# Kernel optimization log

Measured on AMD Instinct MI355X. Metric: run time of the kernel, lower is better.

Reference implementation:

```python
import jax, jax.numpy as jnp
import numpy as np
import math

MAX_ITERATIONS = 10
CONVERGENCE_EPS = 1e-6
B, L = 2048, 2048


def quaternion_normalize(q):
    return q / (jnp.linalg.norm(q, axis=-1, keepdims=True) + 1e-12)


def hamilton_product(q1, q2):
    w1, x1, y1, z1 = q1[..., 0], q1[..., 1], q1[..., 2], q1[..., 3]
    w2, x2, y2, z2 = q2[..., 0], q2[..., 1], q2[..., 2], q2[..., 3]
    return jnp.stack([
        w1 * w2 - x1 * x2 - y1 * y2 - z1 * z2,
        w1 * x2 + x1 * w2 + y1 * z2 - z1 * y2,
        w1 * y2 - x1 * z2 + y1 * w2 + z1 * x2,
        w1 * z2 + x1 * y2 - y1 * x2 + z1 * w2,
    ], axis=-1)


def quaternion_log(q):
    # log map on S^3 at identity
    w = jnp.clip(q[..., 0], -1.0 + 1e-7, 1.0 - 1e-7)
    v = q[..., 1:]
    theta = jnp.arccos(w)
    sin_theta = jnp.sin(theta)[..., None] + 1e-9
    return theta[..., None] / sin_theta * v


def quaternion_exp(v):
    theta = jnp.linalg.norm(v, axis=-1, keepdims=True)
    v_n = v / (theta + 1e-9)
    return jnp.concatenate([jnp.cos(theta), jnp.sin(theta) * v_n], axis=-1)


def compute_karcher_mean(points):
    # points: [N, B, L, 4] unit quaternions
    n = points.shape[0]
    weights = jnp.full((n,), 1.0 / n, dtype=points.dtype)
    conj = jnp.asarray([1.0, -1.0, -1.0, -1.0], dtype=points.dtype)

    def step(carry, _):
        mu, done = carry
        mu_inv = mu * conj
        q_rel = hamilton_product(mu_inv[None], points)      # [N, B, L, 4]
        tangent = quaternion_log(q_rel)                     # [N, B, L, 3]
        mean_v = jnp.sum(tangent * weights[:, None, None, None], axis=0)
        delta_mu = quaternion_exp(mean_v)
        mu_new = quaternion_normalize(hamilton_product(mu, delta_mu))
        # torch: update mu, then break if ||mean_v|| < eps -> freeze afterward
        mu_out = jnp.where(done, mu, mu_new)
        new_done = done | (jnp.linalg.norm(mean_v) < CONVERGENCE_EPS)
        return (mu_out, new_done), None

    mu0 = points[0]
    (mu, _), _ = jax.lax.scan(step, (mu0, jnp.asarray(False)), None, length=MAX_ITERATIONS)
    return mu


def calculate_spectral_shift(barycenter):
    w, x, y, z = (barycenter[..., 0], barycenter[..., 1],
                  barycenter[..., 2], barycenter[..., 3])
    # S = [[w+iz, x+iy], [-x+iy, w-iz]] ; det(S) = (w+iz)(w-iz) - (x+iy)(-x+iy)
    s00 = jax.lax.complex(w, z)
    s01 = jax.lax.complex(x, y)
    s10 = jax.lax.complex(-x, y)
    s11 = jax.lax.complex(w, -z)
    det_s = s00 * s11 - s01 * s10
    return jnp.angle(det_s) / math.pi


def setup_inputs() -> dict:
    key = jax.random.key(0)
    ks = jax.random.split(key, 4)
    names = ['audio', 'vision', 'text', 'genomic']
    return {n: jax.random.normal(k, (B, L, 4), dtype=jnp.float32)
            for n, k in zip(names, ks)}


def reference(audio, vision, text, genomic):
    stacked = jnp.stack([quaternion_normalize(audio),
                         quaternion_normalize(vision),
                         quaternion_normalize(text),
                         quaternion_normalize(genomic)], axis=0)  # [4, B, L, 4]
    barycenter = compute_karcher_mean(stacked)
    eta = calculate_spectral_shift(barycenter)
    curvature = jnp.linalg.norm(barycenter - quaternion_normalize(barycenter))
    veracity = 1.0 / (1.0 + curvature)
    return barycenter, eta, veracity
```

## Files before the change

### kernel.cpp

```cpp
#include <hip/hip_runtime.h>


#define NPTS (2048 * 2048)
#define NBLK (NPTS / 256)

__device__ __forceinline__ float frcp(float x) { return __builtin_amdgcn_rcpf(x); }
__device__ __forceinline__ float frsq(float x) { return __builtin_amdgcn_rsqf(x); }
__device__ __forceinline__ float fsqrt(float x) { return __builtin_amdgcn_sqrtf(x); }

__device__ __forceinline__ float4 qnorm_fast(const float4 q) {
    float inv = frsq(fmaf(q.x, q.x, fmaf(q.y, q.y, fmaf(q.z, q.z, q.w * q.w))));
    return make_float4(q.x * inv, q.y * inv, q.z * inv, q.w * inv);
}

__device__ __forceinline__ float log_scale(float w) {
    float a = fminf(fabsf(w), 0.9999999f);
    float t = fmaf(a, fmaf(a, fmaf(a, -0.004682325f, 0.018565250f), -0.053028600f),
                   0.392682200f);
    float r1 = frsq(1.0f + a);
    float r2 = frsq(1.0f - a);
    float u = fmaf(0.785398163f, r2, -t);
    return r1 * ((w >= 0.0f) ? t : u);
}

__device__ __forceinline__ float sinc_poly(float x) {
    float s = fmaf(x, 1.60590438e-10f, -2.50521084e-8f);
    s = fmaf(x, s, 2.75573192e-6f);
    s = fmaf(x, s, -1.98412698e-4f);
    s = fmaf(x, s, 8.33333333e-3f);
    s = fmaf(x, s, -1.66666667e-1f);
    return fmaf(x, s, 1.0f);
}
__device__ __forceinline__ float cos_poly(float x) {
    float c = fmaf(x, -1.14707456e-11f, 2.08767570e-9f);
    c = fmaf(x, c, -2.75573192e-7f);
    c = fmaf(x, c, 2.48015873e-5f);
    c = fmaf(x, c, -1.38888889e-3f);
    c = fmaf(x, c, 4.16666667e-2f);
    c = fmaf(x, c, -0.5f);
    return fmaf(x, c, 1.0f);
}

__global__ __launch_bounds__(256) void karcher_kernel(
    const float4* __restrict__ aud, const float4* __restrict__ vis,
    const float4* __restrict__ txt, const float4* __restrict__ gen,
    float* __restrict__ out, float* __restrict__ ws)
{
    const int i = blockIdx.x * 256 + threadIdx.x;

    float4 p0 = qnorm_fast(aud[i]);
    float4 p1 = qnorm_fast(vis[i]);
    float4 p2 = qnorm_fast(txt[i]);
    float4 p3 = qnorm_fast(gen[i]);

    float4 mu = p0;

    #pragma unroll
    for (int it = 0; it < 10; ++it) {
        float w0 = fmaf(mu.x, p0.x, fmaf(mu.y, p0.y, fmaf(mu.z, p0.z, mu.w * p0.w)));
        float w1 = fmaf(mu.x, p1.x, fmaf(mu.y, p1.y, fmaf(mu.z, p1.z, mu.w * p1.w)));
        float w2 = fmaf(mu.x, p2.x, fmaf(mu.y, p2.y, fmaf(mu.z, p2.z, mu.w * p2.w)));
        float w3 = fmaf(mu.x, p3.x, fmaf(mu.y, p3.y, fmaf(mu.z, p3.z, mu.w * p3.w)));

        float s0 = log_scale(w0), s1 = log_scale(w1), s2 = log_scale(w2), s3 = log_scale(w3);

        float Tw = fmaf(s0, p0.x, fmaf(s1, p1.x, fmaf(s2, p2.x, s3 * p3.x)));
        float Tx = fmaf(s0, p0.y, fmaf(s1, p1.y, fmaf(s2, p2.y, s3 * p3.y)));
        float Ty = fmaf(s0, p0.z, fmaf(s1, p1.z, fmaf(s2, p2.z, s3 * p3.z)));
        float Tz = fmaf(s0, p0.w, fmaf(s1, p1.w, fmaf(s2, p2.w, s3 * p3.w)));

        float d  = fmaf(mu.x, Tw, fmaf(mu.y, Tx, fmaf(mu.z, Ty, mu.w * Tz)));
        float Ew = fmaf(-d, mu.x, Tw);
        float Ex = fmaf(-d, mu.y, Tx);
        float Ey = fmaf(-d, mu.z, Ty);
        float Ez = fmaf(-d, mu.w, Tz);
        float x  = fmaf(Ew, Ew, fmaf(Ex, Ex, fmaf(Ey, Ey, Ez * Ez)));

        float sc = sinc_poly(x);
        float c  = cos_poly(x);
        mu.x = fmaf(c, mu.x, sc * Ew);
        mu.y = fmaf(c, mu.y, sc * Ex);
        mu.z = fmaf(c, mu.z, sc * Ey);
        mu.w = fmaf(c, mu.w, sc * Ez);
    }

    mu = qnorm_fast(mu);

    reinterpret_cast<float4*>(out)[i] = mu;

    out[4 * NPTS + i] = 0.0f;

    float nn = fmaf(mu.x, mu.x, fmaf(mu.y, mu.y, fmaf(mu.z, mu.z, mu.w * mu.w)));
    float invn = frcp(fsqrt(nn) + 1e-12f);
    float ex = fmaf(-mu.x, invn, mu.x);
    float ey = fmaf(-mu.y, invn, mu.y);
    float ez = fmaf(-mu.z, invn, mu.z);
    float ew = fmaf(-mu.w, invn, mu.w);
    float ss = fmaf(ex, ex, fmaf(ey, ey, fmaf(ez, ez, ew * ew)));

    #pragma unroll
    for (int off = 32; off > 0; off >>= 1)
        ss += __shfl_down(ss, off, 64);
    __shared__ float part[4];
    if ((threadIdx.x & 63) == 0) part[threadIdx.x >> 6] = ss;
    __syncthreads();
    if (threadIdx.x == 0)
        ws[blockIdx.x] = part[0] + part[1] + part[2] + part[3];
}

__global__ __launch_bounds__(256) void finish_kernel(
    const float* __restrict__ ws, float* __restrict__ out)
{
    float s = 0.0f;
    #pragma unroll 4
    for (int k = threadIdx.x; k < NBLK; k += 256)
        s += ws[k];
    #pragma unroll
    for (int off = 32; off > 0; off >>= 1)
        s += __shfl_down(s, off, 64);
    __shared__ float part[4];
    if ((threadIdx.x & 63) == 0) part[threadIdx.x >> 6] = s;
    __syncthreads();
    if (threadIdx.x == 0)
        out[5 * NPTS] = 1.0f / (1.0f + sqrtf(part[0] + part[1] + part[2] + part[3]));
}

extern "C" void kernel_launch(void* const* d_in, const int* in_sizes, int n_in,
                              void* d_out, int out_size, void* d_ws, size_t ws_size,
                              hipStream_t stream) {
    const float4* aud = (const float4*)d_in[0];
    const float4* vis = (const float4*)d_in[1];
    const float4* txt = (const float4*)d_in[2];
    const float4* gen = (const float4*)d_in[3];
    float* out = (float*)d_out;
    float* ws = (float*)d_ws;

    karcher_kernel<<<NBLK, 256, 0, stream>>>(aud, vis, txt, gen, out, ws);
    finish_kernel<<<1, 256, 0, stream>>>(ws, out);
}
```

Before: 145.2 us.

## Process two points per thread, peel first iteration, reuse dot products for tangent projection

```diff
diff --git a/kernel.cpp b/kernel.cpp
--- a/kernel.cpp
+++ b/kernel.cpp
@@ -2,7 +2,7 @@
 
 
 #define NPTS (2048 * 2048)
-#define NBLK (NPTS / 256)
+#define NBLK (NPTS / 512)
 
 __device__ __forceinline__ float frcp(float x) { return __builtin_amdgcn_rcpf(x); }
 __device__ __forceinline__ float frsq(float x) { return __builtin_amdgcn_rsqf(x); }
@@ -41,62 +41,88 @@
     return fmaf(x, c, 1.0f);
 }
 
+__device__ __forceinline__ float4 karcher_update(
+    float4 mu, float s0, float w0,
+    const float4 p0, const float4 p1, const float4 p2, const float4 p3)
+{
+    float w1 = fmaf(mu.x, p1.x, fmaf(mu.y, p1.y, fmaf(mu.z, p1.z, mu.w * p1.w)));
+    float w2 = fmaf(mu.x, p2.x, fmaf(mu.y, p2.y, fmaf(mu.z, p2.z, mu.w * p2.w)));
+    float w3 = fmaf(mu.x, p3.x, fmaf(mu.y, p3.y, fmaf(mu.z, p3.z, mu.w * p3.w)));
+    float s1 = log_scale(w1), s2 = log_scale(w2), s3 = log_scale(w3);
+
+    float Tw = fmaf(s0, p0.x, fmaf(s1, p1.x, fmaf(s2, p2.x, s3 * p3.x)));
+    float Tx = fmaf(s0, p0.y, fmaf(s1, p1.y, fmaf(s2, p2.y, s3 * p3.y)));
+    float Ty = fmaf(s0, p0.z, fmaf(s1, p1.z, fmaf(s2, p2.z, s3 * p3.z)));
+    float Tz = fmaf(s0, p0.w, fmaf(s1, p1.w, fmaf(s2, p2.w, s3 * p3.w)));
+
+    float d = fmaf(s0, w0, fmaf(s1, w1, fmaf(s2, w2, s3 * w3)));
+
+    float Ew = fmaf(-d, mu.x, Tw);
+    float Ex = fmaf(-d, mu.y, Tx);
+    float Ey = fmaf(-d, mu.z, Ty);
+    float Ez = fmaf(-d, mu.w, Tz);
+    float x  = fmaf(Ew, Ew, fmaf(Ex, Ex, fmaf(Ey, Ey, Ez * Ez)));
+
+    float sc = sinc_poly(x);
+    float c  = cos_poly(x);
+    float4 r;
+    r.x = fmaf(c, mu.x, sc * Ew);
+    r.y = fmaf(c, mu.y, sc * Ex);
+    r.z = fmaf(c, mu.z, sc * Ey);
+    r.w = fmaf(c, mu.w, sc * Ez);
+    return r;
+}
+
 __global__ __launch_bounds__(256) void karcher_kernel(
     const float4* __restrict__ aud, const float4* __restrict__ vis,
     const float4* __restrict__ txt, const float4* __restrict__ gen,
     float* __restrict__ out, float* __restrict__ ws)
 {
-    const int i = blockIdx.x * 256 + threadIdx.x;
+    const int i0 = (blockIdx.x * 256 + threadIdx.x) * 2;
 
-    float4 p0 = qnorm_fast(aud[i]);
-    float4 p1 = qnorm_fast(vis[i]);
-    float4 p2 = qnorm_fast(txt[i]);
-    float4 p3 = qnorm_fast(gen[i]);
-
-    float4 mu = p0;
+    float4 p[2][4], mu[2];
+    #pragma unroll
+    for (int j = 0; j < 2; ++j) {
+        p[j][0] = qnorm_fast(aud[i0 + j]);
+        p[j][1] = qnorm_fast(vis[i0 + j]);
+        p[j][2] = qnorm_fast(txt[i0 + j]);
+        p[j][3] = qnorm_fast(gen[i0 + j]);
+    }
 
     #pragma unroll
-    for (int it = 0; it < 10; ++it) {
-        float w0 = fmaf(mu.x, p0.x, fmaf(mu.y, p0.y, fmaf(mu.z, p0.z, mu.w * p0.w)));
-        float w1 = fmaf(mu.x, p1.x, fmaf(mu.y, p1.y, fmaf(mu.z, p1.z, mu.w * p1.w)));
-        float w2 = fmaf(mu.x, p2.x, fmaf(mu.y, p2.y, fmaf(mu.z, p2.z, mu.w * p2.w)));
-        float w3 = fmaf(mu.x, p3.x, fmaf(mu.y, p3.y, fmaf(mu.z, p3.z, mu.w * p3.w)));
+    for (int j = 0; j < 2; ++j)
+        mu[j] = karcher_update(p[j][0], 0.25f, 1.0f,
+                               p[j][0], p[j][1], p[j][2], p[j][3]);
 
-        float s0 = log_scale(w0), s1 = log_scale(w1), s2 = log_scale(w2), s3 = log_scale(w3);
-
-        float Tw = fmaf(s0, p0.x, fmaf(s1, p1.x, fmaf(s2, p2.x, s3 * p3.x)));
-        float Tx = fmaf(s0, p0.y, fmaf(s1, p1.y, fmaf(s2, p2.y, s3 * p3.y)));
-        float Ty = fmaf(s0, p0.z, fmaf(s1, p1.z, fmaf(s2, p2.z, s3 * p3.z)));
-        float Tz = fmaf(s0, p0.w, fmaf(s1, p1.w, fmaf(s2, p2.w, s3 * p3.w)));
-
-        float d  = fmaf(mu.x, Tw, fmaf(mu.y, Tx, fmaf(mu.z, Ty, mu.w * Tz)));
-        float Ew = fmaf(-d, mu.x, Tw);
-        float Ex = fmaf(-d, mu.y, Tx);
-        float Ey = fmaf(-d, mu.z, Ty);
-        float Ez = fmaf(-d, mu.w, Tz);
-        float x  = fmaf(Ew, Ew, fmaf(Ex, Ex, fmaf(Ey, Ey, Ez * Ez)));
-
-        float sc = sinc_poly(x);
-        float c  = cos_poly(x);
-        mu.x = fmaf(c, mu.x, sc * Ew);
-        mu.y = fmaf(c, mu.y, sc * Ex);
-        mu.z = fmaf(c, mu.z, sc * Ey);
-        mu.w = fmaf(c, mu.w, sc * Ez);
+    #pragma unroll 1
+    for (int it = 0; it < 9; ++it) {
+        #pragma unroll
+        for (int j = 0; j < 2; ++j) {
+            float4 m = mu[j];
+            const float4 q0 = p[j][0];
+            float w0 = fmaf(m.x, q0.x, fmaf(m.y, q0.y, fmaf(m.z, q0.z, m.w * q0.w)));
+            float s0 = log_scale(w0);
+            mu[j] = karcher_update(m, s0, w0, q0, p[j][1], p[j][2], p[j][3]);
+        }
     }
 
-    mu = qnorm_fast(mu);
+    float ss = 0.0f;
+    #pragma unroll
+    for (int j = 0; j < 2; ++j) {
+        float4 m = qnorm_fast(mu[j]);
 
-    reinterpret_cast<float4*>(out)[i] = mu;
+        reinterpret_cast<float4*>(out)[i0 + j] = m;
 
-    out[4 * NPTS + i] = 0.0f;
+        out[4 * NPTS + i0 + j] = 0.0f;
 
-    float nn = fmaf(mu.x, mu.x, fmaf(mu.y, mu.y, fmaf(mu.z, mu.z, mu.w * mu.w)));
-    float invn = frcp(fsqrt(nn) + 1e-12f);
-    float ex = fmaf(-mu.x, invn, mu.x);
-    float ey = fmaf(-mu.y, invn, mu.y);
-    float ez = fmaf(-mu.z, invn, mu.z);
-    float ew = fmaf(-mu.w, invn, mu.w);
-    float ss = fmaf(ex, ex, fmaf(ey, ey, fmaf(ez, ez, ew * ew)));
+        float nn = fmaf(m.x, m.x, fmaf(m.y, m.y, fmaf(m.z, m.z, m.w * m.w)));
+        float invn = frcp(fsqrt(nn) + 1e-12f);
+        float ex = fmaf(-m.x, invn, m.x);
+        float ey = fmaf(-m.y, invn, m.y);
+        float ez = fmaf(-m.z, invn, m.z);
+        float ew = fmaf(-m.w, invn, m.w);
+        ss += fmaf(ex, ex, fmaf(ey, ey, fmaf(ez, ez, ew * ew)));
+    }
 
     #pragma unroll
     for (int off = 32; off > 0; off >>= 1)
```

New measurement: 135.1 us. -7.0%, faster.
